# Kernel tuning notes

Measured on AMD Instinct MI355X. Metric: run time of the kernel, lower is better.

Reference implementation:

```python
import jax, jax.numpy as jnp
import numpy as np

N_NODES = 100000
EPS = 1e-12  # F.normalize eps


def _sage_conv(x, src, dst, deg, Wl, bl, Wr):
    # mean aggregation of neighbor (source) features at destination nodes
    agg = jax.ops.segment_sum(x[src], dst, num_segments=N_NODES)  # [N, F]
    agg = agg / jnp.maximum(deg, 1.0)[:, None]
    out = agg @ Wl + bl + x @ Wr  # lin_l(mean(x_j)) + lin_r(x_i)
    # normalize=True -> L2 row normalization
    norm = jnp.sqrt(jnp.sum(out * out, axis=-1, keepdims=True))
    return out / jnp.maximum(norm, EPS)


def setup_inputs() -> dict:
    key = jax.random.key(0)
    ks = jax.random.split(key, 10)
    F_IN, H, C = 14, 32, 2
    x = jax.random.normal(ks[0], (N_NODES, F_IN), dtype=jnp.float32)
    edge_index = jax.random.randint(ks[1], (2, 6400000), 0, N_NODES, dtype=jnp.int32)
    def glorot(k, shape):
        lim = float(np.sqrt(6.0 / (shape[0] + shape[1])))
        return jax.random.uniform(k, shape, jnp.float32, -lim, lim)
    return {
        "x": x,
        "edge_index": edge_index,
        "W1l": glorot(ks[2], (F_IN, H)), "b1": jnp.zeros((H,), jnp.float32),
        "W1r": glorot(ks[3], (F_IN, H)),
        "W2l": glorot(ks[4], (H, H)), "b2": jnp.zeros((H,), jnp.float32),
        "W2r": glorot(ks[5], (H, H)),
        "Wlin": glorot(ks[6], (H, C)), "blin": jnp.zeros((C,), jnp.float32),
    }


def reference(x, edge_index, W1l, b1, W1r, W2l, b2, W2r, Wlin, blin):
    src, dst = edge_index[0], edge_index[1]
    deg = jax.ops.segment_sum(jnp.ones_like(dst, dtype=x.dtype), dst,
                              num_segments=N_NODES)  # in-degree per node
    h = jax.nn.relu(_sage_conv(x, src, dst, deg, W1l, b1, W1r))
    # dropout p=0.2 is identity at inference
    h = jax.nn.relu(_sage_conv(h, src, dst, deg, W2l, b2, W2r))
    return h @ Wlin + blin  # [N, num_classes]
```

## Files before the change

kernel.cpp:

```cpp
#include <hip/hip_runtime.h>
#include <hip/hip_bf16.h>


#define CHA 16384
#define MAXBH 800
#define CAPH 9728

static __device__ __forceinline__ unsigned short f2bf(float f) {
    unsigned u = __float_as_uint(f);
    unsigned r = (u + 0x7FFFu + ((u >> 16) & 1u)) >> 16;
    return (unsigned short)r;
}
#define BF_LO(u) __uint_as_float((u) << 16)
#define BF_HI(u) __uint_as_float((u) & 0xFFFF0000u)

__global__ __launch_bounds__(1024) void partitionA(
        const float* __restrict__ x, unsigned short* __restrict__ xb,
        const int* __restrict__ src, const int* __restrict__ dst,
        int* __restrict__ bcursor, unsigned* __restrict__ part,
        int E, int N, int NBH) {
    __shared__ unsigned pk[CHA];
    __shared__ int h[MAXBH], lofs[MAXBH], delta[MAXBH];
    int t = threadIdx.x;
    int base = blockIdx.x * CHA;
    int end = base + CHA; if (end > E) end = E;
    int cnt = end - base;

    for (int i = blockIdx.x * 1024 + t; i < N * 16; i += gridDim.x * 1024) {
        int n = i >> 4, f = i & 15;
        float v = (f < 14) ? x[n * 14 + f] : 0.f;
        xb[i] = f2bf(v);
    }

    int ed[16], es[16], er[16];
    for (int i = t; i < NBH; i += 1024) h[i] = 0;
    __syncthreads();
    #pragma unroll
    for (int i = 0; i < 4; ++i) {
        int j = i * 4096 + t * 4;
        if (j + 4 <= cnt) {
            int4 d4 = *(const int4*)(dst + base + j);
            int4 s4 = *(const int4*)(src + base + j);
            ed[i*4+0] = d4.x; ed[i*4+1] = d4.y; ed[i*4+2] = d4.z; ed[i*4+3] = d4.w;
            es[i*4+0] = s4.x; es[i*4+1] = s4.y; es[i*4+2] = s4.z; es[i*4+3] = s4.w;
            er[i*4+0] = atomicAdd(&h[d4.x >> 7], 1);
            er[i*4+1] = atomicAdd(&h[d4.y >> 7], 1);
            er[i*4+2] = atomicAdd(&h[d4.z >> 7], 1);
            er[i*4+3] = atomicAdd(&h[d4.w >> 7], 1);
        } else {
            #pragma unroll
            for (int k = 0; k < 4; ++k) {
                if (j + k < cnt) {
                    ed[i*4+k] = dst[base + j + k];
                    es[i*4+k] = src[base + j + k];
                    er[i*4+k] = atomicAdd(&h[ed[i*4+k] >> 7], 1);
                } else ed[i*4+k] = -1;
            }
        }
    }
    __syncthreads();
    if (t < 64) {
        int vals[13];
        int run = 0;
        int b13 = t * 13;
        #pragma unroll
        for (int i = 0; i < 13; ++i) {
            int idx = b13 + i;
            int xv = (idx < NBH) ? h[idx] : 0;
            run += xv;
            vals[i] = run;
        }
        int tot = run, sc = run;
        #pragma unroll
        for (int off = 1; off < 64; off <<= 1) {
            int nv = __shfl_up(sc, off);
            if (t >= off) sc += nv;
        }
        int excl = sc - tot;
        #pragma unroll
        for (int i = 0; i < 13; ++i) {
            int idx = b13 + i;
            if (idx < NBH) {
                h[idx] = excl + vals[i];
                lofs[idx] = excl + (i ? vals[i - 1] : 0);
            }
        }
    }
    __syncthreads();
    if (t < NBH) {
        int excl = lofs[t];
        int v = h[t] - excl;
        int g = v ? atomicAdd(&bcursor[t], v) : 0;
        delta[t] = t * CAPH + g - excl;
    }
    __syncthreads();
    #pragma unroll
    for (int i = 0; i < 16; ++i) {
        int d = ed[i];
        if (d >= 0) {
            int b = d >> 7;
            pk[lofs[b] + er[i]] = ((unsigned)(d & 127) << 24) | (unsigned)es[i];
        }
    }
    __syncthreads();
    int wid = t >> 6, lane = t & 63;
    for (int b = wid; b < NBH; b += 16) {
        int s = lofs[b];
        int e2 = h[b];
        int dlt = delta[b];
        int lim = (b + 1) * CAPH;
        for (int k = s + lane; k < e2; k += 64) {
            int gidx = dlt + k;
            if (gidx < lim) part[gidx] = pk[k];
        }
    }
}

__global__ __launch_bounds__(1024) void partitionB_fused(
        const unsigned* __restrict__ part, const int* __restrict__ bcursor,
        const uint4* __restrict__ xb4, const float* __restrict__ x,
        const float* __restrict__ W1l, const float* __restrict__ b1,
        const float* __restrict__ W1r,
        int* __restrict__ deg, int* __restrict__ offs,
        int* __restrict__ sorted_src, float* __restrict__ hbuf,
        unsigned short* __restrict__ hb, int N, int HALF) {
    __shared__ int pk2[CAPH];
    __shared__ int hh[256], keyofs[256];
    __shared__ int lstart[128], ldeg[128];
    __shared__ float swl[448], swr[448], sb1[32];
    __shared__ int sTot;
    int hbid = blockIdx.x;
    int t = threadIdx.x;
    int start = hbid * CAPH;
    int cc = bcursor[hbid];
    if (cc > CAPH) cc = CAPH;
    int end = start + cc;
    unsigned ce[10];
    int rk[10];
    if (t < 256) hh[t] = 0;
    if (t >= 512 && t < 960) { swl[t - 512] = W1l[t - 512]; swr[t - 512] = W1r[t - 512]; }
    else if (t >= 960 && t < 992) sb1[t - 960] = b1[t - 960];
    __syncthreads();
    #pragma unroll
    for (int i = 0; i < 10; ++i) {
        int idx = start + t + i * 1024;
        unsigned p = 0xFFFFFFFFu;
        int r = 0;
        if (idx < end) {
            p = part[idx];
            int key = (int)(p >> 24) * 2 + (((int)(p & 0xFFFFFFu) < HALF) ? 0 : 1);
            r = atomicAdd(&hh[key], 1);
        }
        ce[i] = p;
        rk[i] = r;
    }
    __syncthreads();
    if (t < 64) {
        int b4 = t * 4;
        int v0 = hh[b4], v1 = hh[b4 + 1], v2 = hh[b4 + 2], v3 = hh[b4 + 3];
        int s1 = v0 + v1, s2 = s1 + v2, s3 = s2 + v3;
        int sc = s3;
        #pragma unroll
        for (int off = 1; off < 64; off <<= 1) {
            int nv = __shfl_up(sc, off);
            if (t >= off) sc += nv;
        }
        int excl = sc - s3;
        keyofs[b4]     = excl;
        keyofs[b4 + 1] = excl + v0;
        keyofs[b4 + 2] = excl + s1;
        keyofs[b4 + 3] = excl + s2;
        if (t == 63) sTot = excl + s3;
    }
    __syncthreads();
    if (t < 128) {
        int lo = hh[2 * t];
        int d = lo + hh[2 * t + 1];
        int excl = keyofs[2 * t];
        lstart[t] = excl;
        ldeg[t] = d;
        int node = hbid * 128 + t;
        if (node < N) {
            deg[node] = d;
            offs[node] = start + excl;
        }
    }
    #pragma unroll
    for (int i = 0; i < 10; ++i) {
        unsigned p = ce[i];
        if (p != 0xFFFFFFFFu) {
            int s = (int)(p & 0xFFFFFFu);
            int key = (int)(p >> 24) * 2 + ((s < HALF) ? 0 : 1);
            int pos = keyofs[key] + rk[i];
            if (pos < CAPH) pk2[pos] = s;
        }
    }
    __syncthreads();
    int tot = sTot; if (tot > CAPH) tot = CAPH;
    for (int i = t; i < tot; i += 1024)
        sorted_src[start + i] = pk2[i];

    int node = t >> 3, sub = t & 7, ep = sub >> 1, half = sub & 1;
    int lanebase = (t & 63) & ~7;
    int gnode = hbid * 128 + node;
    bool valid = gnode < N;
    int js = lstart[node], d = ldeg[node];
    int je = js + d;
    float x0 = 0.f, x1 = 0.f;
    if (valid && sub < 7) {
        x0 = x[gnode * 14 + sub * 2];
        x1 = x[gnode * 14 + sub * 2 + 1];
    }

    float a[8] = {0,0,0,0,0,0,0,0};
    int j = js + ep;
    for (; j + 12 < je; j += 16) {
        int s0 = pk2[j], s1 = pk2[j + 4], s2 = pk2[j + 8], s3 = pk2[j + 12];
        uint4 u0 = xb4[s0 * 2 + half], u1 = xb4[s1 * 2 + half];
        uint4 u2 = xb4[s2 * 2 + half], u3 = xb4[s3 * 2 + half];
        a[0] += (BF_LO(u0.x) + BF_LO(u1.x)) + (BF_LO(u2.x) + BF_LO(u3.x));
        a[1] += (BF_HI(u0.x) + BF_HI(u1.x)) + (BF_HI(u2.x) + BF_HI(u3.x));
        a[2] += (BF_LO(u0.y) + BF_LO(u1.y)) + (BF_LO(u2.y) + BF_LO(u3.y));
        a[3] += (BF_HI(u0.y) + BF_HI(u1.y)) + (BF_HI(u2.y) + BF_HI(u3.y));
        a[4] += (BF_LO(u0.z) + BF_LO(u1.z)) + (BF_LO(u2.z) + BF_LO(u3.z));
        a[5] += (BF_HI(u0.z) + BF_HI(u1.z)) + (BF_HI(u2.z) + BF_HI(u3.z));
        a[6] += (BF_LO(u0.w) + BF_LO(u1.w)) + (BF_LO(u2.w) + BF_LO(u3.w));
        a[7] += (BF_HI(u0.w) + BF_HI(u1.w)) + (BF_HI(u2.w) + BF_HI(u3.w));
    }
    for (; j + 4 < je; j += 8) {
        int s0 = pk2[j], s1 = pk2[j + 4];
        uint4 u0 = xb4[s0 * 2 + half], u1 = xb4[s1 * 2 + half];
        a[0] += BF_LO(u0.x) + BF_LO(u1.x);
        a[1] += BF_HI(u0.x) + BF_HI(u1.x);
        a[2] += BF_LO(u0.y) + BF_LO(u1.y);
        a[3] += BF_HI(u0.y) + BF_HI(u1.y);
        a[4] += BF_LO(u0.z) + BF_LO(u1.z);
        a[5] += BF_HI(u0.z) + BF_HI(u1.z);
        a[6] += BF_LO(u0.w) + BF_LO(u1.w);
        a[7] += BF_HI(u0.w) + BF_HI(u1.w);
    }
    for (; j < je; j += 4) {
        uint4 u0 = xb4[pk2[j] * 2 + half];
        a[0] += BF_LO(u0.x); a[1] += BF_HI(u0.x);
        a[2] += BF_LO(u0.y); a[3] += BF_HI(u0.y);
        a[4] += BF_LO(u0.z); a[5] += BF_HI(u0.z);
        a[6] += BF_LO(u0.w); a[7] += BF_HI(u0.w);
    }
    #pragma unroll
    for (int i = 0; i < 8; ++i) {
        a[i] += __shfl_xor(a[i], 2);
        a[i] += __shfl_xor(a[i], 4);
    }

    float inv = 1.0f / ((d > 0) ? (float)d : 1.0f);
    float acc[4];
    #pragma unroll
    for (int i = 0; i < 4; ++i) acc[i] = sb1[sub * 4 + i];
    #pragma unroll
    for (int k = 0; k < 14; ++k) {
        float ag = __shfl(a[k & 7], lanebase + (k >> 3)) * inv;
        float xv = __shfl((k & 1) ? x1 : x0, lanebase + (k >> 1));
        float4 wl = *(const float4*)&swl[k * 32 + sub * 4];
        float4 wr = *(const float4*)&swr[k * 32 + sub * 4];
        acc[0] += ag * wl.x + xv * wr.x;
        acc[1] += ag * wl.y + xv * wr.y;
        acc[2] += ag * wl.z + xv * wr.z;
        acc[3] += ag * wl.w + xv * wr.w;
    }
    float ss = 0.f;
    #pragma unroll
    for (int i = 0; i < 4; ++i) ss += acc[i] * acc[i];
    ss += __shfl_xor(ss, 1); ss += __shfl_xor(ss, 2); ss += __shfl_xor(ss, 4);
    float invn = 1.f / fmaxf(sqrtf(ss), 1e-12f);
    if (valid) {
        float hv[4];
        #pragma unroll
        for (int i = 0; i < 4; ++i) hv[i] = fmaxf(acc[i] * invn, 0.f);
        *(float4*)(hbuf + (size_t)gnode * 32 + sub * 4) =
            make_float4(hv[0], hv[1], hv[2], hv[3]);
        uint2 pb;
        pb.x = (unsigned)f2bf(hv[0]) | ((unsigned)f2bf(hv[1]) << 16);
        pb.y = (unsigned)f2bf(hv[2]) | ((unsigned)f2bf(hv[3]) << 16);
        *(uint2*)(hb + (size_t)gnode * 32 + sub * 4) = pb;
    }
}

__global__ __launch_bounds__(256) void gather32_dense2(
        const uint4* __restrict__ hb, const int* __restrict__ sorted_src,
        const int* __restrict__ offs, const int* __restrict__ deg,
        const float* __restrict__ hbuf,
        const float* __restrict__ W2l, const float* __restrict__ b2,
        const float* __restrict__ W2r, const float* __restrict__ Wlin,
        const float* __restrict__ blin, float* __restrict__ out, int N) {
    __shared__ float sa[64 * 33];
    __shared__ float sh2[64 * 33];
    __shared__ float swl[1024], swr[1024], swo[64], sb[32], sbo[2];
    int t = threadIdx.x;
    for (int i = t; i < 1024; i += 256) { swl[i] = W2l[i]; swr[i] = W2r[i]; }
    if (t < 64) swo[t] = Wlin[t];
    if (t < 32) sb[t] = b2[t];
    if (t < 2) sbo[t] = blin[t];

    int row = t >> 2, q = t & 3;
    int n = blockIdx.x * 64 + row;
    bool valid = n < N;
    int start = valid ? offs[n] : 0;
    int d = valid ? deg[n] : 0;
    float a0=0,a1=0,a2=0,a3=0,a4=0,a5=0,a6=0,a7=0;
    int j = 0;
    for (; j + 8 <= d; j += 8) {
        int s0 = sorted_src[start + j + 0];
        int s1 = sorted_src[start + j + 1];
        int s2 = sorted_src[start + j + 2];
        int s3 = sorted_src[start + j + 3];
        int s4 = sorted_src[start + j + 4];
        int s5 = sorted_src[start + j + 5];
        int s6 = sorted_src[start + j + 6];
        int s7 = sorted_src[start + j + 7];
        uint4 u0 = hb[s0 * 4 + q];
        uint4 u1 = hb[s1 * 4 + q];
        uint4 u2 = hb[s2 * 4 + q];
        uint4 u3 = hb[s3 * 4 + q];
        uint4 u4 = hb[s4 * 4 + q];
        uint4 u5 = hb[s5 * 4 + q];
        uint4 u6 = hb[s6 * 4 + q];
        uint4 u7 = hb[s7 * 4 + q];
        a0 += (BF_LO(u0.x)+BF_LO(u1.x)+BF_LO(u2.x)+BF_LO(u3.x))
            + (BF_LO(u4.x)+BF_LO(u5.x)+BF_LO(u6.x)+BF_LO(u7.x));
        a1 += (BF_HI(u0.x)+BF_HI(u1.x)+BF_HI(u2.x)+BF_HI(u3.x))
            + (BF_HI(u4.x)+BF_HI(u5.x)+BF_HI(u6.x)+BF_HI(u7.x));
        a2 += (BF_LO(u0.y)+BF_LO(u1.y)+BF_LO(u2.y)+BF_LO(u3.y))
            + (BF_LO(u4.y)+BF_LO(u5.y)+BF_LO(u6.y)+BF_LO(u7.y));
        a3 += (BF_HI(u0.y)+BF_HI(u1.y)+BF_HI(u2.y)+BF_HI(u3.y))
            + (BF_HI(u4.y)+BF_HI(u5.y)+BF_HI(u6.y)+BF_HI(u7.y));
        a4 += (BF_LO(u0.z)+BF_LO(u1.z)+BF_LO(u2.z)+BF_LO(u3.z))
            + (BF_LO(u4.z)+BF_LO(u5.z)+BF_LO(u6.z)+BF_LO(u7.z));
        a5 += (BF_HI(u0.z)+BF_HI(u1.z)+BF_HI(u2.z)+BF_HI(u3.z))
            + (BF_HI(u4.z)+BF_HI(u5.z)+BF_HI(u6.z)+BF_HI(u7.z));
        a6 += (BF_LO(u0.w)+BF_LO(u1.w)+BF_LO(u2.w)+BF_LO(u3.w))
            + (BF_LO(u4.w)+BF_LO(u5.w)+BF_LO(u6.w)+BF_LO(u7.w));
        a7 += (BF_HI(u0.w)+BF_HI(u1.w)+BF_HI(u2.w)+BF_HI(u3.w))
            + (BF_HI(u4.w)+BF_HI(u5.w)+BF_HI(u6.w)+BF_HI(u7.w));
    }
    for (; j + 4 <= d; j += 4) {
        int s0 = sorted_src[start + j + 0];
        int s1 = sorted_src[start + j + 1];
        int s2 = sorted_src[start + j + 2];
        int s3 = sorted_src[start + j + 3];
        uint4 u0 = hb[s0 * 4 + q];
        uint4 u1 = hb[s1 * 4 + q];
        uint4 u2 = hb[s2 * 4 + q];
        uint4 u3 = hb[s3 * 4 + q];
        a0 += BF_LO(u0.x)+BF_LO(u1.x)+BF_LO(u2.x)+BF_LO(u3.x);
        a1 += BF_HI(u0.x)+BF_HI(u1.x)+BF_HI(u2.x)+BF_HI(u3.x);
        a2 += BF_LO(u0.y)+BF_LO(u1.y)+BF_LO(u2.y)+BF_LO(u3.y);
        a3 += BF_HI(u0.y)+BF_HI(u1.y)+BF_HI(u2.y)+BF_HI(u3.y);
        a4 += BF_LO(u0.z)+BF_LO(u1.z)+BF_LO(u2.z)+BF_LO(u3.z);
        a5 += BF_HI(u0.z)+BF_HI(u1.z)+BF_HI(u2.z)+BF_HI(u3.z);
        a6 += BF_LO(u0.w)+BF_LO(u1.w)+BF_LO(u2.w)+BF_LO(u3.w);
        a7 += BF_HI(u0.w)+BF_HI(u1.w)+BF_HI(u2.w)+BF_HI(u3.w);
    }
    for (; j < d; ++j) {
        uint4 u0 = hb[sorted_src[start + j] * 4 + q];
        a0 += BF_LO(u0.x); a1 += BF_HI(u0.x);
        a2 += BF_LO(u0.y); a3 += BF_HI(u0.y);
        a4 += BF_LO(u0.z); a5 += BF_HI(u0.z);
        a6 += BF_LO(u0.w); a7 += BF_HI(u0.w);
    }
    if (valid) {
        float inv = 1.0f / ((d > 0) ? (float)d : 1.0f);
        float* sd = &sa[row * 33 + q * 8];
        sd[0] = a0 * inv; sd[1] = a1 * inv; sd[2] = a2 * inv; sd[3] = a3 * inv;
        sd[4] = a4 * inv; sd[5] = a5 * inv; sd[6] = a6 * inv; sd[7] = a7 * inv;
        const float4* gh = (const float4*)(hbuf + (size_t)n * 32 + q * 8);
        float4 h0 = gh[0], h1 = gh[1];
        float* se = &sh2[row * 33 + q * 8];
        se[0] = h0.x; se[1] = h0.y; se[2] = h0.z; se[3] = h0.w;
        se[4] = h1.x; se[5] = h1.y; se[6] = h1.z; se[7] = h1.w;
    }
    __syncthreads();

    float acc[8];
    #pragma unroll
    for (int i = 0; i < 8; ++i) acc[i] = sb[q * 8 + i];
    for (int k = 0; k < 32; ++k) {
        float av = sa[row * 33 + k];
        float hv = sh2[row * 33 + k];
        const float4* wl4 = (const float4*)&swl[k * 32 + q * 8];
        const float4* wr4 = (const float4*)&swr[k * 32 + q * 8];
        float4 wla = wl4[0], wlb = wl4[1], wra = wr4[0], wrb = wr4[1];
        acc[0] += av * wla.x + hv * wra.x;
        acc[1] += av * wla.y + hv * wra.y;
        acc[2] += av * wla.z + hv * wra.z;
        acc[3] += av * wla.w + hv * wra.w;
        acc[4] += av * wlb.x + hv * wrb.x;
        acc[5] += av * wlb.y + hv * wrb.y;
        acc[6] += av * wlb.z + hv * wrb.z;
        acc[7] += av * wlb.w + hv * wrb.w;
    }
    float ss = 0.f;
    #pragma unroll
    for (int i = 0; i < 8; ++i) ss += acc[i] * acc[i];
    ss += __shfl_xor(ss, 1); ss += __shfl_xor(ss, 2);
    float invn = 1.f / fmaxf(sqrtf(ss), 1e-12f);
    float o0 = 0.f, o1 = 0.f;
    #pragma unroll
    for (int i = 0; i < 8; ++i) {
        float hv = fmaxf(acc[i] * invn, 0.f);
        int kk = q * 8 + i;
        o0 += hv * swo[kk * 2 + 0];
        o1 += hv * swo[kk * 2 + 1];
    }
    o0 += __shfl_xor(o0, 1); o0 += __shfl_xor(o0, 2);
    o1 += __shfl_xor(o1, 1); o1 += __shfl_xor(o1, 2);
    if (q == 0 && valid) {
        out[n * 2 + 0] = o0 + sbo[0];
        out[n * 2 + 1] = o1 + sbo[1];
    }
}

extern "C" void kernel_launch(void* const* d_in, const int* in_sizes, int n_in,
                              void* d_out, int out_size, void* d_ws, size_t ws_size,
                              hipStream_t stream) {
    const float* x    = (const float*)d_in[0];
    const int*   ei   = (const int*)d_in[1];
    const float* W1l  = (const float*)d_in[2];
    const float* b1   = (const float*)d_in[3];
    const float* W1r  = (const float*)d_in[4];
    const float* W2l  = (const float*)d_in[5];
    const float* b2   = (const float*)d_in[6];
    const float* W2r  = (const float*)d_in[7];
    const float* Wlin = (const float*)d_in[8];
    const float* blin = (const float*)d_in[9];
    float* out = (float*)d_out;

    const int N = in_sizes[0] / 14;
    const int E = in_sizes[1] / 2;
    const int* src = ei;
    const int* dst = ei + E;
    const int NBH = (N + 127) / 128;
    const int HALF = N / 2;

    char* ws = (char*)d_ws;
    size_t off = 0;
    auto alloc = [&](size_t bytes) -> void* {
        void* p = ws + off;
        off = (off + bytes + 255) & ~(size_t)255;
        return p;
    };
    int*            bcursor    = (int*)alloc((size_t)NBH * 4);
    unsigned*       part       = (unsigned*)alloc((size_t)NBH * CAPH * 4);
    int*            sorted_src = (int*)alloc((size_t)NBH * CAPH * 4);
    int*            deg        = (int*)alloc((size_t)N * 4);
    int*            offs       = (int*)alloc((size_t)N * 4);
    unsigned short* xb         = (unsigned short*)alloc((size_t)N * 16 * 2);
    float*          hbuf       = (float*)alloc((size_t)N * 32 * 4);
    unsigned short* hb         = (unsigned short*)alloc((size_t)N * 32 * 2);
    (void)ws_size; (void)n_in; (void)out_size;

    hipMemsetAsync(bcursor, 0, (size_t)NBH * 4, stream);
    partitionA<<<(E + CHA - 1) / CHA, 1024, 0, stream>>>(
        x, xb, src, dst, bcursor, part, E, N, NBH);
    partitionB_fused<<<NBH, 1024, 0, stream>>>(
        part, bcursor, (const uint4*)xb, x, W1l, b1, W1r,
        deg, offs, sorted_src, hbuf, hb, N, HALF);
    gather32_dense2<<<(N + 63) / 64, 256, 0, stream>>>(
        (const uint4*)hb, sorted_src, offs, deg, hbuf,
        W2l, b2, W2r, Wlin, blin, out, N);
}
```

Measured before the change: 266.0 us.

## Use nontemporal loads/stores for streams and phase the layer-2 gather by source half

```diff
diff --git a/kernel.cpp b/kernel.cpp
--- a/kernel.cpp
+++ b/kernel.cpp
@@ -5,6 +5,10 @@
 #define CHA 16384
 #define MAXBH 800
 #define CAPH 9728
+
+typedef int      vi4 __attribute__((ext_vector_type(4)));
+typedef float    vf4 __attribute__((ext_vector_type(4)));
+typedef unsigned vu2 __attribute__((ext_vector_type(2)));
 
 static __device__ __forceinline__ unsigned short f2bf(float f) {
     unsigned u = __float_as_uint(f);
@@ -13,6 +17,7 @@
 }
 #define BF_LO(u) __uint_as_float((u) << 16)
 #define BF_HI(u) __uint_as_float((u) & 0xFFFF0000u)
+#define NTL(p) __builtin_nontemporal_load(p)
 
 __global__ __launch_bounds__(1024) void partitionA(
         const float* __restrict__ x, unsigned short* __restrict__ xb,
@@ -39,8 +44,8 @@
     for (int i = 0; i < 4; ++i) {
         int j = i * 4096 + t * 4;
         if (j + 4 <= cnt) {
-            int4 d4 = *(const int4*)(dst + base + j);
-            int4 s4 = *(const int4*)(src + base + j);
+            vi4 d4 = NTL((const vi4*)(dst + base + j));
+            vi4 s4 = NTL((const vi4*)(src + base + j));
             ed[i*4+0] = d4.x; ed[i*4+1] = d4.y; ed[i*4+2] = d4.z; ed[i*4+3] = d4.w;
             es[i*4+0] = s4.x; es[i*4+1] = s4.y; es[i*4+2] = s4.z; es[i*4+3] = s4.w;
             er[i*4+0] = atomicAdd(&h[d4.x >> 7], 1);
@@ -111,7 +116,7 @@
         int lim = (b + 1) * CAPH;
         for (int k = s + lane; k < e2; k += 64) {
             int gidx = dlt + k;
-            if (gidx < lim) part[gidx] = pk[k];
+            if (gidx < lim) __builtin_nontemporal_store(pk[k], &part[gidx]);
         }
     }
 }
@@ -121,7 +126,7 @@
         const uint4* __restrict__ xb4, const float* __restrict__ x,
         const float* __restrict__ W1l, const float* __restrict__ b1,
         const float* __restrict__ W1r,
-        int* __restrict__ deg, int* __restrict__ offs,
+        int* __restrict__ deg, int* __restrict__ offs, int* __restrict__ nlo,
         int* __restrict__ sorted_src, float* __restrict__ hbuf,
         unsigned short* __restrict__ hb, int N, int HALF) {
     __shared__ int pk2[CAPH];
@@ -147,7 +152,7 @@
         unsigned p = 0xFFFFFFFFu;
         int r = 0;
         if (idx < end) {
-            p = part[idx];
+            p = NTL(&part[idx]);
             int key = (int)(p >> 24) * 2 + (((int)(p & 0xFFFFFFu) < HALF) ? 0 : 1);
             r = atomicAdd(&hh[key], 1);
         }
@@ -183,6 +188,7 @@
         if (node < N) {
             deg[node] = d;
             offs[node] = start + excl;
+            nlo[node] = lo;
         }
     }
     #pragma unroll
@@ -198,7 +204,7 @@
     __syncthreads();
     int tot = sTot; if (tot > CAPH) tot = CAPH;
     for (int i = t; i < tot; i += 1024)
-        sorted_src[start + i] = pk2[i];
+        __builtin_nontemporal_store(pk2[i], &sorted_src[start + i]);
 
     int node = t >> 3, sub = t & 7, ep = sub >> 1, half = sub & 1;
     int lanebase = (t & 63) & ~7;
@@ -276,19 +282,19 @@
         float hv[4];
         #pragma unroll
         for (int i = 0; i < 4; ++i) hv[i] = fmaxf(acc[i] * invn, 0.f);
-        *(float4*)(hbuf + (size_t)gnode * 32 + sub * 4) =
-            make_float4(hv[0], hv[1], hv[2], hv[3]);
-        uint2 pb;
+        vf4 hv4 = { hv[0], hv[1], hv[2], hv[3] };
+        __builtin_nontemporal_store(hv4, (vf4*)(hbuf + (size_t)gnode * 32 + sub * 4));
+        vu2 pb;
         pb.x = (unsigned)f2bf(hv[0]) | ((unsigned)f2bf(hv[1]) << 16);
         pb.y = (unsigned)f2bf(hv[2]) | ((unsigned)f2bf(hv[3]) << 16);
-        *(uint2*)(hb + (size_t)gnode * 32 + sub * 4) = pb;
+        __builtin_nontemporal_store(pb, (vu2*)(hb + (size_t)gnode * 32 + sub * 4));
     }
 }
 
 __global__ __launch_bounds__(256) void gather32_dense2(
         const uint4* __restrict__ hb, const int* __restrict__ sorted_src,
         const int* __restrict__ offs, const int* __restrict__ deg,
-        const float* __restrict__ hbuf,
+        const int* __restrict__ nlo, const float* __restrict__ hbuf,
         const float* __restrict__ W2l, const float* __restrict__ b2,
         const float* __restrict__ W2r, const float* __restrict__ Wlin,
         const float* __restrict__ blin, float* __restrict__ out, int N) {
@@ -306,74 +312,65 @@
     bool valid = n < N;
     int start = valid ? offs[n] : 0;
     int d = valid ? deg[n] : 0;
+    int dlo = valid ? nlo[n] : 0;
     float a0=0,a1=0,a2=0,a3=0,a4=0,a5=0,a6=0,a7=0;
+
+#define G32_BODY(JEND)                                                        \
+    for (; j + 8 <= (JEND); j += 8) {                                         \
+        int s0 = NTL(&sorted_src[start + j + 0]);                             \
+        int s1 = NTL(&sorted_src[start + j + 1]);                             \
+        int s2 = NTL(&sorted_src[start + j + 2]);                             \
+        int s3 = NTL(&sorted_src[start + j + 3]);                             \
+        int s4 = NTL(&sorted_src[start + j + 4]);                             \
+        int s5 = NTL(&sorted_src[start + j + 5]);                             \
+        int s6 = NTL(&sorted_src[start + j + 6]);                             \
+        int s7 = NTL(&sorted_src[start + j + 7]);                             \
+        uint4 u0 = hb[s0 * 4 + q];                                            \
+        uint4 u1 = hb[s1 * 4 + q];                                            \
+        uint4 u2 = hb[s2 * 4 + q];                                            \
+        uint4 u3 = hb[s3 * 4 + q];                                            \
+        uint4 u4 = hb[s4 * 4 + q];                                            \
+        uint4 u5 = hb[s5 * 4 + q];                                            \
+        uint4 u6 = hb[s6 * 4 + q];                                            \
+        uint4 u7 = hb[s7 * 4 + q];                                            \
+        a0 += (BF_LO(u0.x)+BF_LO(u1.x)+BF_LO(u2.x)+BF_LO(u3.x))               \
+            + (BF_LO(u4.x)+BF_LO(u5.x)+BF_LO(u6.x)+BF_LO(u7.x));              \
+        a1 += (BF_HI(u0.x)+BF_HI(u1.x)+BF_HI(u2.x)+BF_HI(u3.x))               \
+            + (BF_HI(u4.x)+BF_HI(u5.x)+BF_HI(u6.x)+BF_HI(u7.x));              \
+        a2 += (BF_LO(u0.y)+BF_LO(u1.y)+BF_LO(u2.y)+BF_LO(u3.y))               \
+            + (BF_LO(u4.y)+BF_LO(u5.y)+BF_LO(u6.y)+BF_LO(u7.y));              \
+        a3 += (BF_HI(u0.y)+BF_HI(u1.y)+BF_HI(u2.y)+BF_HI(u3.y))               \
+            + (BF_HI(u4.y)+BF_HI(u5.y)+BF_HI(u6.y)+BF_HI(u7.y));              \
+        a4 += (BF_LO(u0.z)+BF_LO(u1.z)+BF_LO(u2.z)+BF_LO(u3.z))               \
+            + (BF_LO(u4.z)+BF_LO(u5.z)+BF_LO(u6.z)+BF_LO(u7.z));              \
+        a5 += (BF_HI(u0.z)+BF_HI(u1.z)+BF_HI(u2.z)+BF_HI(u3.z))               \
+            + (BF_HI(u4.z)+BF_HI(u5.z)+BF_HI(u6.z)+BF_HI(u7.z));              \
+        a6 += (BF_LO(u0.w)+BF_LO(u1.w)+BF_LO(u2.w)+BF_LO(u3.w))               \
+            + (BF_LO(u4.w)+BF_LO(u5.w)+BF_LO(u6.w)+BF_LO(u7.w));              \
+        a7 += (BF_HI(u0.w)+BF_HI(u1.w)+BF_HI(u2.w)+BF_HI(u3.w))               \
+            + (BF_HI(u4.w)+BF_HI(u5.w)+BF_HI(u6.w)+BF_HI(u7.w));              \
+    }                                                                         \
+    for (; j < (JEND); ++j) {                                                 \
+        uint4 u0 = hb[NTL(&sorted_src[start + j]) * 4 + q];                   \
+        a0 += BF_LO(u0.x); a1 += BF_HI(u0.x);                                 \
+        a2 += BF_LO(u0.y); a3 += BF_HI(u0.y);                                 \
+        a4 += BF_LO(u0.z); a5 += BF_HI(u0.z);                                 \
+        a6 += BF_LO(u0.w); a7 += BF_HI(u0.w);                                 \
+    }
+
     int j = 0;
-    for (; j + 8 <= d; j += 8) {
-        int s0 = sorted_src[start + j + 0];
-        int s1 = sorted_src[start + j + 1];
-        int s2 = sorted_src[start + j + 2];
-        int s3 = sorted_src[start + j + 3];
-        int s4 = sorted_src[start + j + 4];
-        int s5 = sorted_src[start + j + 5];
-        int s6 = sorted_src[start + j + 6];
-        int s7 = sorted_src[start + j + 7];
-        uint4 u0 = hb[s0 * 4 + q];
-        uint4 u1 = hb[s1 * 4 + q];
-        uint4 u2 = hb[s2 * 4 + q];
-        uint4 u3 = hb[s3 * 4 + q];
-        uint4 u4 = hb[s4 * 4 + q];
-        uint4 u5 = hb[s5 * 4 + q];
-        uint4 u6 = hb[s6 * 4 + q];
-        uint4 u7 = hb[s7 * 4 + q];
-        a0 += (BF_LO(u0.x)+BF_LO(u1.x)+BF_LO(u2.x)+BF_LO(u3.x))
-            + (BF_LO(u4.x)+BF_LO(u5.x)+BF_LO(u6.x)+BF_LO(u7.x));
-        a1 += (BF_HI(u0.x)+BF_HI(u1.x)+BF_HI(u2.x)+BF_HI(u3.x))
-            + (BF_HI(u4.x)+BF_HI(u5.x)+BF_HI(u6.x)+BF_HI(u7.x));
-        a2 += (BF_LO(u0.y)+BF_LO(u1.y)+BF_LO(u2.y)+BF_LO(u3.y))
-            + (BF_LO(u4.y)+BF_LO(u5.y)+BF_LO(u6.y)+BF_LO(u7.y));
-        a3 += (BF_HI(u0.y)+BF_HI(u1.y)+BF_HI(u2.y)+BF_HI(u3.y))
-            + (BF_HI(u4.y)+BF_HI(u5.y)+BF_HI(u6.y)+BF_HI(u7.y));
-        a4 += (BF_LO(u0.z)+BF_LO(u1.z)+BF_LO(u2.z)+BF_LO(u3.z))
-            + (BF_LO(u4.z)+BF_LO(u5.z)+BF_LO(u6.z)+BF_LO(u7.z));
-        a5 += (BF_HI(u0.z)+BF_HI(u1.z)+BF_HI(u2.z)+BF_HI(u3.z))
-            + (BF_HI(u4.z)+BF_HI(u5.z)+BF_HI(u6.z)+BF_HI(u7.z));
-        a6 += (BF_LO(u0.w)+BF_LO(u1.w)+BF_LO(u2.w)+BF_LO(u3.w))
-            + (BF_LO(u4.w)+BF_LO(u5.w)+BF_LO(u6.w)+BF_LO(u7.w));
-        a7 += (BF_HI(u0.w)+BF_HI(u1.w)+BF_HI(u2.w)+BF_HI(u3.w))
-            + (BF_HI(u4.w)+BF_HI(u5.w)+BF_HI(u6.w)+BF_HI(u7.w));
-    }
-    for (; j + 4 <= d; j += 4) {
-        int s0 = sorted_src[start + j + 0];
-        int s1 = sorted_src[start + j + 1];
-        int s2 = sorted_src[start + j + 2];
-        int s3 = sorted_src[start + j + 3];
-        uint4 u0 = hb[s0 * 4 + q];
-        uint4 u1 = hb[s1 * 4 + q];
-        uint4 u2 = hb[s2 * 4 + q];
-        uint4 u3 = hb[s3 * 4 + q];
-        a0 += BF_LO(u0.x)+BF_LO(u1.x)+BF_LO(u2.x)+BF_LO(u3.x);
-        a1 += BF_HI(u0.x)+BF_HI(u1.x)+BF_HI(u2.x)+BF_HI(u3.x);
-        a2 += BF_LO(u0.y)+BF_LO(u1.y)+BF_LO(u2.y)+BF_LO(u3.y);
-        a3 += BF_HI(u0.y)+BF_HI(u1.y)+BF_HI(u2.y)+BF_HI(u3.y);
-        a4 += BF_LO(u0.z)+BF_LO(u1.z)+BF_LO(u2.z)+BF_LO(u3.z);
-        a5 += BF_HI(u0.z)+BF_HI(u1.z)+BF_HI(u2.z)+BF_HI(u3.z);
-        a6 += BF_LO(u0.w)+BF_LO(u1.w)+BF_LO(u2.w)+BF_LO(u3.w);
-        a7 += BF_HI(u0.w)+BF_HI(u1.w)+BF_HI(u2.w)+BF_HI(u3.w);
-    }
-    for (; j < d; ++j) {
-        uint4 u0 = hb[sorted_src[start + j] * 4 + q];
-        a0 += BF_LO(u0.x); a1 += BF_HI(u0.x);
-        a2 += BF_LO(u0.y); a3 += BF_HI(u0.y);
-        a4 += BF_LO(u0.z); a5 += BF_HI(u0.z);
-        a6 += BF_LO(u0.w); a7 += BF_HI(u0.w);
-    }
+    G32_BODY(dlo)
+    __syncthreads();
+    G32_BODY(d)
+#undef G32_BODY
+
     if (valid) {
         float inv = 1.0f / ((d > 0) ? (float)d : 1.0f);
         float* sd = &sa[row * 33 + q * 8];
         sd[0] = a0 * inv; sd[1] = a1 * inv; sd[2] = a2 * inv; sd[3] = a3 * inv;
         sd[4] = a4 * inv; sd[5] = a5 * inv; sd[6] = a6 * inv; sd[7] = a7 * inv;
-        const float4* gh = (const float4*)(hbuf + (size_t)n * 32 + q * 8);
-        float4 h0 = gh[0], h1 = gh[1];
+        const vf4* gh = (const vf4*)(hbuf + (size_t)n * 32 + q * 8);
+        vf4 h0 = NTL(gh), h1 = NTL(gh + 1);
         float* se = &sh2[row * 33 + q * 8];
         se[0] = h0.x; se[1] = h0.y; se[2] = h0.z; se[3] = h0.w;
         se[4] = h1.x; se[5] = h1.y; se[6] = h1.z; se[7] = h1.w;
@@ -453,18 +450,19 @@
     int*            sorted_src = (int*)alloc((size_t)NBH * CAPH * 4);
     int*            deg        = (int*)alloc((size_t)N * 4);
     int*            offs       = (int*)alloc((size_t)N * 4);
+    int*            nlo        = (int*)alloc((size_t)N * 4);
     unsigned short* xb         = (unsigned short*)alloc((size_t)N * 16 * 2);
     float*          hbuf       = (float*)alloc((size_t)N * 32 * 4);
     unsigned short* hb         = (unsigned short*)alloc((size_t)N * 32 * 2);
     (void)ws_size; (void)n_in; (void)out_size;
 
-    hipMemsetAsync(bcursor, 0, (size_t)NBH * 4, stream);
+    (void)hipMemsetAsync(bcursor, 0, (size_t)NBH * 4, stream);
     partitionA<<<(E + CHA - 1) / CHA, 1024, 0, stream>>>(
         x, xb, src, dst, bcursor, part, E, N, NBH);
     partitionB_fused<<<NBH, 1024, 0, stream>>>(
         part, bcursor, (const uint4*)xb, x, W1l, b1, W1r,
-        deg, offs, sorted_src, hbuf, hb, N, HALF);
+        deg, offs, nlo, sorted_src, hbuf, hb, N, HALF);
     gather32_dense2<<<(N + 63) / 64, 256, 0, stream>>>(
-        (const uint4*)hb, sorted_src, offs, deg, hbuf,
+        (const uint4*)hb, sorted_src, offs, deg, nlo, hbuf,
         W2l, b2, W2r, Wlin, blin, out, N);
 }
```

Result: slower. 283.1 us (+6.4%).
